# Performance work log

Hardware: AMD Instinct MI355X
Metric: run time of the kernel (lower is better)

## Reference

```python
import jax, jax.numpy as jnp
import numpy as np

N_NODES = 50000
N_EDGES = 800000
IN_DIM, HID_DIM, LAT_DIM = 512, 512, 128


def _glorot(key, shape):
    fan_in = shape[0]
    return jax.random.normal(key, shape, dtype=jnp.float32) / np.sqrt(fan_in)


def setup_inputs() -> dict:
    key = jax.random.key(0)
    ks = jax.random.split(key, 10)
    x = jax.random.normal(ks[0], (N_NODES, IN_DIM), dtype=jnp.float32)
    edge_index = jax.random.randint(ks[1], (2, N_EDGES), 0, N_NODES, dtype=jnp.int64)
    edge_weight = jax.random.uniform(ks[2], (N_EDGES,), dtype=jnp.float32)
    return {
        "x": x,
        "edge_index": edge_index,
        "edge_weight": edge_weight,
        "W1": _glorot(ks[3], (IN_DIM, HID_DIM)), "b1": jnp.zeros((HID_DIM,), jnp.float32),
        "W2": _glorot(ks[4], (HID_DIM, LAT_DIM)), "b2": jnp.zeros((LAT_DIM,), jnp.float32),
        "W3": _glorot(ks[5], (LAT_DIM, HID_DIM)), "b3": jnp.zeros((HID_DIM,), jnp.float32),
        "W4": _glorot(ks[6], (HID_DIM, IN_DIM)), "b4": jnp.zeros((IN_DIM,), jnp.float32),
    }


def gcn_conv(x, W, b, src, dst, ew, n_nodes):
    """PyG GCNConv: out = D^{-1/2}(A+I)D^{-1/2} X W + b, self-loop weight 1."""
    xw = x @ W  # [N, out_dim]
    # degree over edges + self-loops (self-loop weight = 1)
    deg = jax.ops.segment_sum(ew, dst, num_segments=n_nodes) + 1.0  # [N]
    dinv = jnp.where(deg > 0, jax.lax.rsqrt(deg), 0.0)
    norm = dinv[src] * ew * dinv[dst]  # [E]
    msg = norm[:, None] * xw[src]      # [E, out_dim] per-edge gather
    agg = jax.ops.segment_sum(msg, dst, num_segments=n_nodes)  # scatter-add
    agg = agg + (dinv * dinv)[:, None] * xw  # self-loop contribution
    return agg + b


def reference(x, edge_index, edge_weight, W1, b1, W2, b2, W3, b3, W4, b4):
    src, dst = edge_index[0], edge_index[1]
    n = x.shape[0]
    # encode
    h = jax.nn.relu(gcn_conv(x, W1, b1, src, dst, edge_weight, n))
    z = gcn_conv(h, W2, b2, src, dst, edge_weight, n)
    # decode (dropout is identity in eval mode)
    h2 = jax.nn.relu(gcn_conv(z, W3, b3, src, dst, edge_weight, n))
    x_recon = gcn_conv(h2, W4, b4, src, dst, edge_weight, n)
    return (x_recon, z)
```

## Files before the change

### kernel.cpp

```cpp
#include <hip/hip_runtime.h>


typedef short bf16x8 __attribute__((ext_vector_type(8)));
typedef float f32x4 __attribute__((ext_vector_type(4)));

__device__ __forceinline__ float bf2f(unsigned short u) {
  return __uint_as_float(((unsigned int)u) << 16);
}
__device__ __forceinline__ unsigned short f2bf(float f) {
  unsigned int u = __float_as_uint(f);
  return (unsigned short)((u + 0x7fffu + ((u >> 16) & 1u)) >> 16);
}

__device__ __forceinline__ void gload_lds16(const void* g, void* l) {
  __builtin_amdgcn_global_load_lds(
      (const __attribute__((address_space(1))) unsigned int*)g,
      (__attribute__((address_space(3))) unsigned int*)l, 16, 0, 0);
}


__global__ void deg_hist_kernel(const int* __restrict__ dst, const float* __restrict__ ew,
                                float* __restrict__ deg, int* __restrict__ cnt, int E) {
  int e = blockIdx.x * blockDim.x + threadIdx.x;
  if (e >= E) return;
  int d = dst[e];
  atomicAdd(&deg[d], ew[e]);
  atomicAdd(&cnt[d], 1);
}

__global__ void dinv_kernel(const float* __restrict__ deg, float* __restrict__ dinv, int n) {
  int i = blockIdx.x * blockDim.x + threadIdx.x;
  if (i >= n) return;
  dinv[i] = rsqrtf(deg[i] + 1.0f);
}

__global__ void block_sums_kernel(const int* __restrict__ cnt, int* __restrict__ sums, int n) {
  __shared__ int sh[512];
  int i = blockIdx.x * 512 + threadIdx.x;
  sh[threadIdx.x] = (i < n) ? cnt[i] : 0;
  __syncthreads();
  for (int s = 256; s > 0; s >>= 1) {
    if (threadIdx.x < s) sh[threadIdx.x] += sh[threadIdx.x + s];
    __syncthreads();
  }
  if (threadIdx.x == 0) sums[blockIdx.x] = sh[0];
}

__global__ void scan_sums_kernel(int* sums, int nb) {
  if (threadIdx.x == 0 && blockIdx.x == 0) {
    int acc = 0;
    for (int i = 0; i < nb; ++i) { int v = sums[i]; sums[i] = acc; acc += v; }
  }
}

__global__ void scan_final_kernel(const int* __restrict__ cnt, const int* __restrict__ sums,
                                  int* __restrict__ rowPtr, int* __restrict__ fill, int n) {
  __shared__ int sh[512];
  int i = blockIdx.x * 512 + threadIdx.x;
  int v = (i < n) ? cnt[i] : 0;
  sh[threadIdx.x] = v;
  __syncthreads();
  for (int off = 1; off < 512; off <<= 1) {
    int y = (threadIdx.x >= off) ? sh[threadIdx.x - off] : 0;
    __syncthreads();
    sh[threadIdx.x] += y;
    __syncthreads();
  }
  if (i < n) {
    int incl = sh[threadIdx.x];
    int base = sums[blockIdx.x];
    int excl = base + incl - v;
    rowPtr[i] = excl;
    fill[i] = excl;
    if (i == n - 1) rowPtr[n] = base + incl;
  }
}

__global__ void scatter_edges_kernel(const int* __restrict__ src, const int* __restrict__ dst,
                                     const float* __restrict__ ew, const float* __restrict__ dinv,
                                     int* __restrict__ fill, int* __restrict__ col,
                                     float* __restrict__ val, int E) {
  int e = blockIdx.x * blockDim.x + threadIdx.x;
  if (e >= E) return;
  int s = src[e], d = dst[e];
  int p = atomicAdd(&fill[d], 1);
  col[p] = s;
  val[p] = dinv[s] * ew[e] * dinv[d];
}


__global__ void cvt_x_kernel(const float* __restrict__ x, unsigned short* __restrict__ xbf,
                             int n, int Mpad) {
  int g = blockIdx.x * 256 + threadIdx.x;
  int total = Mpad * 64;
  if (g >= total) return;
  int row = g >> 6;
  int cc = (g & 63) << 3;
  bf16x8 o;
  if (row < n) {
    const float* p = x + (size_t)row * 512 + cc;
    float4 f0 = *(const float4*)p;
    float4 f1 = *(const float4*)(p + 4);
    o[0] = (short)f2bf(f0.x); o[1] = (short)f2bf(f0.y);
    o[2] = (short)f2bf(f0.z); o[3] = (short)f2bf(f0.w);
    o[4] = (short)f2bf(f1.x); o[5] = (short)f2bf(f1.y);
    o[6] = (short)f2bf(f1.z); o[7] = (short)f2bf(f1.w);
  } else {
#pragma unroll
    for (int j = 0; j < 8; ++j) o[j] = 0;
  }
  *(bf16x8*)(xbf + (size_t)g * 8) = o;
}


__global__ void tile_w_kernel(const float* __restrict__ W, short* __restrict__ hi,
                              int K, int N) {
  int g = blockIdx.x * 256 + threadIdx.x;
  int kb_cnt = K >> 6;
  int total = (N >> 7) * kb_cnt * 1024;
  if (g >= total) return;
  int c = g & 1023;
  int t = g >> 10;
  int kb = t % kb_cnt;
  int nb = t / kb_cnt;
  int colg = (nb << 7) + (c >> 3);
  int k0 = (kb << 6) + (((c & 7) ^ ((c >> 3) & 7)) << 3);
  bf16x8 h8;
#pragma unroll
  for (int j = 0; j < 8; ++j) {
    float w = W[(size_t)(k0 + j) * N + colg];
    h8[j] = (short)f2bf(w);
  }
  *(bf16x8*)(hi + (size_t)g * 8) = h8;
}


template <bool BIAS, bool RELU>
__global__ __launch_bounds__(256) void mfma_gemm(
    const unsigned short* __restrict__ A, const short* __restrict__ Bhi,
    const float* __restrict__ bias, unsigned short* __restrict__ C, int N, int K) {
  __shared__ short As[8192];
  __shared__ short Bh[8192];
  const int tid = threadIdx.x;
  const int lane = tid & 63;
  const int wave = tid >> 6;
  const int rowblk = blockIdx.y << 7;
  const int colblk = blockIdx.x << 7;
  const int wr = ((wave >> 1) << 6);
  const int wc = ((wave & 1) << 6);
  const int lr = lane & 15;
  const int lk = lane >> 4;
  const int kbN = K >> 6;

  f32x4 acc[4][4];
#pragma unroll
  for (int i = 0; i < 4; ++i)
#pragma unroll
    for (int j = 0; j < 4; ++j) {
      f32x4 z = {0.f, 0.f, 0.f, 0.f};
      acc[i][j] = z;
    }

  const int arow = wave * 32 + (lane >> 3);
  const size_t abase = (size_t)(rowblk + arow) * K + (size_t)(((lane & 7) ^ (lane >> 3)) << 3);
  const size_t btile0 = ((size_t)(colblk >> 7) * kbN) << 13;
  const int bchunk = wave * 256 + lane;

  short* AsW = As + wave * 2048;
  short* BhW = Bh + wave * 2048;

  for (int kb = 0; kb < kbN; ++kb) {
    const unsigned short* asrc = A + abase + (kb << 6);
    const short* bhsrc = Bhi + btile0 + ((size_t)kb << 13) + (size_t)bchunk * 8;
#pragma unroll
    for (int i = 0; i < 4; ++i) {
      gload_lds16(asrc + (size_t)(i * 8) * K, AsW + i * 512);
      gload_lds16(bhsrc + i * 512, BhW + i * 512);
    }
    __syncthreads();
#pragma unroll
    for (int kk = 0; kk < 2; ++kk) {
      bf16x8 af[4], bhf[4];
      const int kc = kk * 4 + lk;
#pragma unroll
      for (int rb = 0; rb < 4; ++rb) {
        int rowl = wr + rb * 16 + lr;
        af[rb] = *(const bf16x8*)(As + rowl * 64 + ((kc ^ (rowl & 7)) << 3));
      }
#pragma unroll
      for (int cb = 0; cb < 4; ++cb) {
        int coll = wc + cb * 16 + lr;
        bhf[cb] = *(const bf16x8*)(Bh + coll * 64 + ((kc ^ (coll & 7)) << 3));
      }
#pragma unroll
      for (int rb = 0; rb < 4; ++rb)
#pragma unroll
        for (int cb = 0; cb < 4; ++cb)
          acc[rb][cb] = __builtin_amdgcn_mfma_f32_16x16x32_bf16(af[rb], bhf[cb], acc[rb][cb], 0, 0, 0);
    }
    __syncthreads();
  }

#pragma unroll
  for (int cb = 0; cb < 4; ++cb) {
    int colg = colblk + wc + cb * 16 + lr;
    float badd = BIAS ? bias[colg] : 0.0f;
#pragma unroll
    for (int rb = 0; rb < 4; ++rb) {
#pragma unroll
      for (int i = 0; i < 4; ++i) {
        int row = rowblk + wr + rb * 16 + lk * 4 + i;
        float v = acc[rb][cb][i] + badd;
        if (RELU) v = fmaxf(v, 0.f);
        C[(size_t)row * N + colg] = f2bf(v);
      }
    }
  }
}


template <int PT, bool INF32>
__device__ __forceinline__ void load_row(const void* p, size_t off, float* xv) {
  if (INF32) {
    if (PT == 2) {
      float2 f = *(const float2*)((const float*)p + off);
      xv[0] = f.x; xv[1] = f.y;
    } else {
      float4 f0 = *(const float4*)((const float*)p + off);
      float4 f1 = *(const float4*)((const float*)p + off + 4);
      xv[0] = f0.x; xv[1] = f0.y; xv[2] = f0.z; xv[3] = f0.w;
      xv[4] = f1.x; xv[5] = f1.y; xv[6] = f1.z; xv[7] = f1.w;
    }
  } else {
    if (PT == 2) {
      unsigned int u = *(const unsigned int*)((const unsigned short*)p + off);
      xv[0] = bf2f((unsigned short)(u & 0xffffu));
      xv[1] = bf2f((unsigned short)(u >> 16));
    } else {
      bf16x8 r = *(const bf16x8*)((const short*)p + off);
#pragma unroll
      for (int j = 0; j < 8; ++j) xv[j] = bf2f((unsigned short)r[j]);
    }
  }
}

template <int PT, bool INF32, bool BIAS, bool RELU, bool W32, bool W16>
__global__ __launch_bounds__(256) void agg_kernel(
    const void* __restrict__ xw, const int* __restrict__ col, const float* __restrict__ val,
    const int* __restrict__ rowPtr, const float* __restrict__ dinv,
    const float* __restrict__ bias, float* __restrict__ out32,
    unsigned short* __restrict__ out16, int n) {
  const int DIM = PT * 64;
  int node = blockIdx.x * 4 + (threadIdx.x >> 6);
  if (node >= n) return;
  int t = threadIdx.x & 63;
  float acc[PT];
#pragma unroll
  for (int q = 0; q < PT; ++q) acc[q] = 0.f;

  int beg = rowPtr[node], end = rowPtr[node + 1];
  int e = beg;
  for (; e + 4 <= end; e += 4) {
    int s0 = col[e + 0], s1 = col[e + 1], s2 = col[e + 2], s3 = col[e + 3];
    float v0 = val[e + 0], v1 = val[e + 1], v2 = val[e + 2], v3 = val[e + 3];
    float x0[PT], x1[PT], x2[PT], x3[PT];
    load_row<PT, INF32>(xw, (size_t)s0 * DIM + t * PT, x0);
    load_row<PT, INF32>(xw, (size_t)s1 * DIM + t * PT, x1);
    load_row<PT, INF32>(xw, (size_t)s2 * DIM + t * PT, x2);
    load_row<PT, INF32>(xw, (size_t)s3 * DIM + t * PT, x3);
#pragma unroll
    for (int q = 0; q < PT; ++q)
      acc[q] += v0 * x0[q] + v1 * x1[q] + v2 * x2[q] + v3 * x3[q];
  }
  for (; e < end; ++e) {
    int s = col[e];
    float v = val[e];
    float xv[PT];
    load_row<PT, INF32>(xw, (size_t)s * DIM + t * PT, xv);
#pragma unroll
    for (int q = 0; q < PT; ++q) acc[q] += v * xv[q];
  }
  float di = dinv[node];
  float sl = di * di;
  {
    float xv[PT];
    load_row<PT, INF32>(xw, (size_t)node * DIM + t * PT, xv);
#pragma unroll
    for (int q = 0; q < PT; ++q) acc[q] += sl * xv[q];
  }
  if (BIAS) {
#pragma unroll
    for (int q = 0; q < PT; ++q) acc[q] += bias[t * PT + q];
  }
  if (RELU) {
#pragma unroll
    for (int q = 0; q < PT; ++q) acc[q] = fmaxf(acc[q], 0.f);
  }
  if (W32) {
    if (PT == 2) {
      float2 o; o.x = acc[0]; o.y = acc[1];
      *(float2*)(out32 + (size_t)node * DIM + t * PT) = o;
    } else {
      float4 o0, o1;
      o0.x = acc[0]; o0.y = acc[1]; o0.z = acc[2]; o0.w = acc[3];
      o1.x = acc[4 % PT]; o1.y = acc[5 % PT]; o1.z = acc[6 % PT]; o1.w = acc[7 % PT];
      *(float4*)(out32 + (size_t)node * DIM + t * PT) = o0;
      *(float4*)(out32 + (size_t)node * DIM + t * PT + 4) = o1;
    }
  }
  if (W16) {
    if (PT == 2) {
      unsigned int u = (unsigned int)f2bf(acc[0]) | ((unsigned int)f2bf(acc[1]) << 16);
      *(unsigned int*)(out16 + (size_t)node * DIM + t * PT) = u;
    } else {
      bf16x8 o;
#pragma unroll
      for (int j = 0; j < PT; ++j) o[j % 8] = (short)f2bf(acc[j]);
      *(bf16x8*)(out16 + (size_t)node * DIM + t * PT) = o;
    }
  }
}


extern "C" void kernel_launch(void* const* d_in, const int* in_sizes, int n_in,
                              void* d_out, int out_size, void* d_ws, size_t ws_size,
                              hipStream_t stream) {
  const float* x  = (const float*)d_in[0];
  const int*   ei = (const int*)d_in[1];
  const float* ew = (const float*)d_in[2];
  const float* W1 = (const float*)d_in[3];
  const float* b1 = (const float*)d_in[4];
  const float* W2 = (const float*)d_in[5];
  const float* b2 = (const float*)d_in[6];
  const float* W3 = (const float*)d_in[7];
  const float* b3 = (const float*)d_in[8];
  const float* W4 = (const float*)d_in[9];
  const float* b4 = (const float*)d_in[10];

  const int n = in_sizes[0] / 512;
  const int E = in_sizes[2];
  const int MB128 = (n + 127) / 128;
  const int Mpad = MB128 * 128;

  float* out   = (float*)d_out;
  float* z_out = out + (size_t)n * 512;

  char* w = (char*)d_ws;
  auto alloc = [&](size_t bytes) {
    char* p = w;
    w += (bytes + 255) & ~(size_t)255;
    return p;
  };
  float* deg    = (float*)alloc((size_t)n * 4);
  float* dinv   = (float*)alloc((size_t)n * 4);
  int*   cnt    = (int*)alloc((size_t)n * 4);
  int*   rowPtr = (int*)alloc((size_t)(n + 1) * 4);
  int*   fill   = (int*)alloc((size_t)n * 4);
  int*   sums   = (int*)alloc(4096);
  int*   col    = (int*)alloc((size_t)E * 4);
  float* val    = (float*)alloc((size_t)E * 4);
  short* whi1 = (short*)alloc((size_t)512 * 512 * 2);
  short* whi2 = (short*)alloc((size_t)512 * 128 * 2);
  short* whi3 = (short*)alloc((size_t)128 * 512 * 2);
  short* whi4 = (short*)alloc((size_t)512 * 512 * 2);
  unsigned short* T  = (unsigned short*)alloc((size_t)Mpad * 128 * 2);
  unsigned short* B1 = (unsigned short*)alloc((size_t)Mpad * 512 * 2);
  unsigned short* B2 = (unsigned short*)alloc((size_t)Mpad * 512 * 2);

  unsigned short* zbf = B2;

  const int* srcp = ei;
  const int* dstp = ei + E;

  hipMemsetAsync(deg, 0, (size_t)n * 4, stream);
  hipMemsetAsync(cnt, 0, (size_t)n * 4, stream);
  deg_hist_kernel<<<(E + 255) / 256, 256, 0, stream>>>(dstp, ew, deg, cnt, E);
  dinv_kernel<<<(n + 255) / 256, 256, 0, stream>>>(deg, dinv, n);
  int NB = (n + 511) / 512;
  block_sums_kernel<<<NB, 512, 0, stream>>>(cnt, sums, n);
  scan_sums_kernel<<<1, 64, 0, stream>>>(sums, NB);
  scan_final_kernel<<<NB, 512, 0, stream>>>(cnt, sums, rowPtr, fill, n);
  scatter_edges_kernel<<<(E + 255) / 256, 256, 0, stream>>>(srcp, dstp, ew, dinv, fill, col, val, E);

  tile_w_kernel<<<(4 * 8 * 1024 + 255) / 256, 256, 0, stream>>>(W1, whi1, 512, 512);
  tile_w_kernel<<<(1 * 8 * 1024 + 255) / 256, 256, 0, stream>>>(W2, whi2, 512, 128);
  tile_w_kernel<<<(4 * 2 * 1024 + 255) / 256, 256, 0, stream>>>(W3, whi3, 128, 512);
  tile_w_kernel<<<(4 * 8 * 1024 + 255) / 256, 256, 0, stream>>>(W4, whi4, 512, 512);
  cvt_x_kernel<<<(Mpad * 64 + 255) / 256, 256, 0, stream>>>(x, B1, n, Mpad);

  const int AGB = (n + 3) / 4;

  mfma_gemm<false, false><<<dim3(4, MB128), 256, 0, stream>>>(B1, whi1, nullptr, B2, 512, 512);
  agg_kernel<8, false, true, true, false, true><<<AGB, 256, 0, stream>>>(
      B2, col, val, rowPtr, dinv, b1, nullptr, B1, n);

  mfma_gemm<false, false><<<dim3(1, MB128), 256, 0, stream>>>(B1, whi2, nullptr, T, 128, 512);
  agg_kernel<2, false, true, false, true, true><<<AGB, 256, 0, stream>>>(
      T, col, val, rowPtr, dinv, b2, z_out, zbf, n);

  agg_kernel<2, false, false, false, false, true><<<AGB, 256, 0, stream>>>(
      zbf, col, val, rowPtr, dinv, nullptr, nullptr, T, n);
  mfma_gemm<true, true><<<dim3(4, MB128), 256, 0, stream>>>(T, whi3, b3, B2, 512, 128);

  mfma_gemm<false, false><<<dim3(4, MB128), 256, 0, stream>>>(B2, whi4, nullptr, B1, 512, 512);
  agg_kernel<8, false, true, false, true, false><<<AGB, 256, 0, stream>>>(
      B1, col, val, rowPtr, dinv, b4, out, nullptr, n);
}
```

Measured before the change: 667.9 us.

## Widen GEMM column tile to 256 and pack CSR col/val into int2

The MFMA GEMM is templated on column tile width. The N=512 GEMMs now use 256-wide tiles with 512 threads, so each A tile loaded into LDS is reused across twice as many output columns, halving redundant A reads. Separately, the CSR column index and edge weight are packed into a single int2 array, so the aggregation kernels fetch both with one 8-byte load per edge instead of two scattered 4-byte loads. Larger blocks use more LDS (48KB) and may reduce occupancy.

Result: faster. 640.8 us (-4.1%).

```diff
diff --git a/kernel.cpp b/kernel.cpp
--- a/kernel.cpp
+++ b/kernel.cpp
@@ -78,14 +78,13 @@
 
 __global__ void scatter_edges_kernel(const int* __restrict__ src, const int* __restrict__ dst,
                                      const float* __restrict__ ew, const float* __restrict__ dinv,
-                                     int* __restrict__ fill, int* __restrict__ col,
-                                     float* __restrict__ val, int E) {
+                                     int* __restrict__ fill, int2* __restrict__ pk, int E) {
   int e = blockIdx.x * blockDim.x + threadIdx.x;
   if (e >= E) return;
   int s = src[e], d = dst[e];
   int p = atomicAdd(&fill[d], 1);
-  col[p] = s;
-  val[p] = dinv[s] * ew[e] * dinv[d];
+  float v = dinv[s] * ew[e] * dinv[d];
+  pk[p] = make_int2(s, __float_as_int(v));
 }
 
 
@@ -135,22 +134,33 @@
 }
 
 
-template <bool BIAS, bool RELU>
-__global__ __launch_bounds__(256) void mfma_gemm(
+template <int BN, bool BIAS, bool RELU>
+__global__ __launch_bounds__(2 * BN) void mfma_gemm(
     const unsigned short* __restrict__ A, const short* __restrict__ Bhi,
     const float* __restrict__ bias, unsigned short* __restrict__ C, int N, int K) {
+  constexpr int W = BN / 32;
+  constexpr int RW = 128 / W;
+  constexpr int IA = RW / 8;
+  constexpr int NH = BN / 128;
+  constexpr int WH = W / NH;
+  constexpr int CW = BN / 64;
+
   __shared__ short As[8192];
-  __shared__ short Bh[8192];
+  __shared__ short Bs[BN * 64];
+
   const int tid = threadIdx.x;
   const int lane = tid & 63;
   const int wave = tid >> 6;
   const int rowblk = blockIdx.y << 7;
-  const int colblk = blockIdx.x << 7;
-  const int wr = ((wave >> 1) << 6);
-  const int wc = ((wave & 1) << 6);
+  const int colblk = blockIdx.x * BN;
+  const int wr = (wave / CW) << 6;
+  const int wc = (wave % CW) << 6;
   const int lr = lane & 15;
   const int lk = lane >> 4;
   const int kbN = K >> 6;
+  const int half = wave / WH;
+  const int wh = wave % WH;
+  const int nb0 = colblk >> 7;
 
   f32x4 acc[4][4];
 #pragma unroll
@@ -161,22 +171,20 @@
       acc[i][j] = z;
     }
 
-  const int arow = wave * 32 + (lane >> 3);
-  const size_t abase = (size_t)(rowblk + arow) * K + (size_t)(((lane & 7) ^ (lane >> 3)) << 3);
-  const size_t btile0 = ((size_t)(colblk >> 7) * kbN) << 13;
-  const int bchunk = wave * 256 + lane;
-
-  short* AsW = As + wave * 2048;
-  short* BhW = Bh + wave * 2048;
+  const int arow = wave * RW + (lane >> 3);
+  const size_t abase = (size_t)(rowblk + arow) * K + (size_t)(((lane & 7) ^ ((lane >> 3) & 7)) << 3);
+  short* AsW = As + wave * (RW * 64);
+  short* BsW = Bs + half * 8192 + wh * 2048;
 
   for (int kb = 0; kb < kbN; ++kb) {
     const unsigned short* asrc = A + abase + (kb << 6);
-    const short* bhsrc = Bhi + btile0 + ((size_t)kb << 13) + (size_t)bchunk * 8;
-#pragma unroll
-    for (int i = 0; i < 4; ++i) {
+    const short* bsrc = Bhi + ((size_t)(nb0 + half) * kbN + kb) * 8192 + (size_t)(wh * 256 + lane) * 8;
+#pragma unroll
+    for (int i = 0; i < IA; ++i)
       gload_lds16(asrc + (size_t)(i * 8) * K, AsW + i * 512);
-      gload_lds16(bhsrc + i * 512, BhW + i * 512);
-    }
+#pragma unroll
+    for (int i = 0; i < 4; ++i)
+      gload_lds16(bsrc + i * 512, BsW + i * 512);
     __syncthreads();
 #pragma unroll
     for (int kk = 0; kk < 2; ++kk) {
@@ -190,7 +198,7 @@
 #pragma unroll
       for (int cb = 0; cb < 4; ++cb) {
         int coll = wc + cb * 16 + lr;
-        bhf[cb] = *(const bf16x8*)(Bh + coll * 64 + ((kc ^ (coll & 7)) << 3));
+        bhf[cb] = *(const bf16x8*)(Bs + coll * 64 + ((kc ^ (coll & 7)) << 3));
       }
 #pragma unroll
       for (int rb = 0; rb < 4; ++rb)
@@ -246,7 +254,7 @@
 
 template <int PT, bool INF32, bool BIAS, bool RELU, bool W32, bool W16>
 __global__ __launch_bounds__(256) void agg_kernel(
-    const void* __restrict__ xw, const int* __restrict__ col, const float* __restrict__ val,
+    const void* __restrict__ xw, const int2* __restrict__ pk,
     const int* __restrict__ rowPtr, const float* __restrict__ dinv,
     const float* __restrict__ bias, float* __restrict__ out32,
     unsigned short* __restrict__ out16, int n) {
@@ -261,22 +269,23 @@
   int beg = rowPtr[node], end = rowPtr[node + 1];
   int e = beg;
   for (; e + 4 <= end; e += 4) {
-    int s0 = col[e + 0], s1 = col[e + 1], s2 = col[e + 2], s3 = col[e + 3];
-    float v0 = val[e + 0], v1 = val[e + 1], v2 = val[e + 2], v3 = val[e + 3];
+    int2 p0 = pk[e + 0], p1 = pk[e + 1], p2 = pk[e + 2], p3 = pk[e + 3];
     float x0[PT], x1[PT], x2[PT], x3[PT];
-    load_row<PT, INF32>(xw, (size_t)s0 * DIM + t * PT, x0);
-    load_row<PT, INF32>(xw, (size_t)s1 * DIM + t * PT, x1);
-    load_row<PT, INF32>(xw, (size_t)s2 * DIM + t * PT, x2);
-    load_row<PT, INF32>(xw, (size_t)s3 * DIM + t * PT, x3);
+    load_row<PT, INF32>(xw, (size_t)p0.x * DIM + t * PT, x0);
+    load_row<PT, INF32>(xw, (size_t)p1.x * DIM + t * PT, x1);
+    load_row<PT, INF32>(xw, (size_t)p2.x * DIM + t * PT, x2);
+    load_row<PT, INF32>(xw, (size_t)p3.x * DIM + t * PT, x3);
+    float v0 = __int_as_float(p0.y), v1 = __int_as_float(p1.y);
+    float v2 = __int_as_float(p2.y), v3 = __int_as_float(p3.y);
 #pragma unroll
     for (int q = 0; q < PT; ++q)
       acc[q] += v0 * x0[q] + v1 * x1[q] + v2 * x2[q] + v3 * x3[q];
   }
   for (; e < end; ++e) {
-    int s = col[e];
-    float v = val[e];
+    int2 pe = pk[e];
+    float v = __int_as_float(pe.y);
     float xv[PT];
-    load_row<PT, INF32>(xw, (size_t)s * DIM + t * PT, xv);
+    load_row<PT, INF32>(xw, (size_t)pe.x * DIM + t * PT, xv);
 #pragma unroll
     for (int q = 0; q < PT; ++q) acc[q] += v * xv[q];
   }
@@ -357,8 +366,7 @@
   int*   rowPtr = (int*)alloc((size_t)(n + 1) * 4);
   int*   fill   = (int*)alloc((size_t)n * 4);
   int*   sums   = (int*)alloc(4096);
-  int*   col    = (int*)alloc((size_t)E * 4);
-  float* val    = (float*)alloc((size_t)E * 4);
+  int2*  pk     = (int2*)alloc((size_t)E * 8);
   short* whi1 = (short*)alloc((size_t)512 * 512 * 2);
   short* whi2 = (short*)alloc((size_t)512 * 128 * 2);
   short* whi3 = (short*)alloc((size_t)128 * 512 * 2);
@@ -380,7 +388,7 @@
   block_sums_kernel<<<NB, 512, 0, stream>>>(cnt, sums, n);
   scan_sums_kernel<<<1, 64, 0, stream>>>(sums, NB);
   scan_final_kernel<<<NB, 512, 0, stream>>>(cnt, sums, rowPtr, fill, n);
-  scatter_edges_kernel<<<(E + 255) / 256, 256, 0, stream>>>(srcp, dstp, ew, dinv, fill, col, val, E);
+  scatter_edges_kernel<<<(E + 255) / 256, 256, 0, stream>>>(srcp, dstp, ew, dinv, fill, pk, E);
 
   tile_w_kernel<<<(4 * 8 * 1024 + 255) / 256, 256, 0, stream>>>(W1, whi1, 512, 512);
   tile_w_kernel<<<(1 * 8 * 1024 + 255) / 256, 256, 0, stream>>>(W2, whi2, 512, 128);
@@ -390,19 +398,19 @@
 
   const int AGB = (n + 3) / 4;
 
-  mfma_gemm<false, false><<<dim3(4, MB128), 256, 0, stream>>>(B1, whi1, nullptr, B2, 512, 512);
+  mfma_gemm<256, false, false><<<dim3(2, MB128), 512, 0, stream>>>(B1, whi1, nullptr, B2, 512, 512);
   agg_kernel<8, false, true, true, false, true><<<AGB, 256, 0, stream>>>(
-      B2, col, val, rowPtr, dinv, b1, nullptr, B1, n);
-
-  mfma_gemm<false, false><<<dim3(1, MB128), 256, 0, stream>>>(B1, whi2, nullptr, T, 128, 512);
+      B2, pk, rowPtr, dinv, b1, nullptr, B1, n);
+
+  mfma_gemm<128, false, false><<<dim3(1, MB128), 256, 0, stream>>>(B1, whi2, nullptr, T, 128, 512);
   agg_kernel<2, false, true, false, true, true><<<AGB, 256, 0, stream>>>(
-      T, col, val, rowPtr, dinv, b2, z_out, zbf, n);
+      T, pk, rowPtr, dinv, b2, z_out, zbf, n);
 
   agg_kernel<2, false, false, false, false, true><<<AGB, 256, 0, stream>>>(
-      zbf, col, val, rowPtr, dinv, nullptr, nullptr, T, n);
-  mfma_gemm<true, true><<<dim3(4, MB128), 256, 0, stream>>>(T, whi3, b3, B2, 512, 128);
-
-  mfma_gemm<false, false><<<dim3(4, MB128), 256, 0, stream>>>(B2, whi4, nullptr, B1, 512, 512);
+      zbf, pk, rowPtr, dinv, nullptr, nullptr, T, n);
+  mfma_gemm<256, true, true><<<dim3(2, MB128), 512, 0, stream>>>(T, whi3, b3, B2, 512, 128);
+
+  mfma_gemm<256, false, false><<<dim3(2, MB128), 512, 0, stream>>>(B2, whi4, nullptr, B1, 512, 512);
   agg_kernel<8, false, true, false, true, false><<<AGB, 256, 0, stream>>>(
-      B1, col, val, rowPtr, dinv, b4, out, nullptr, n);
-}
+      B1, pk, rowPtr, dinv, b4, out, nullptr, n);
+}
```
